# Kernel optimization log

Measured on AMD Instinct MI355X. Metric: run time of the kernel, lower is better.

## Reference

```python
import jax, jax.numpy as jnp
import numpy as np

B, H, W = 4, 128, 128
THRESHOLD = 0.1      # hard-coded in chamfer_distance_batch
CHUNK = 2048         # row-chunk size for the online-min over the distance matrix
BIG = 1e9            # masks out inactive columns in the min-reduction
EMPTY_CHD = 1e6      # sentinel when either point set is empty (matches torch code)
EPS = 1e-12          # sqrt clamp for numerical safety


def setup_inputs() -> dict:
    key = jax.random.key(0)
    k1, k2 = jax.random.split(key)
    batch1 = jax.random.normal(k1, (B, H, W), dtype=jnp.float32)
    batch2 = jax.random.normal(k2, (B, H, W), dtype=jnp.float32)
    return {"batch1": batch1, "batch2": batch2}


def _chamfer(batch1, batch2):
    Bn, Hn, Wn = batch1.shape
    HW = Hn * Wn
    w1 = jax.nn.relu(batch1 - THRESHOLD).reshape(Bn, HW)   # [B, HW]
    w2 = jax.nn.relu(batch2 - THRESHOLD).reshape(Bn, HW)
    gy, gx = jnp.meshgrid(jnp.arange(Hn), jnp.arange(Wn), indexing='ij')
    coords = jnp.stack([gy, gx], axis=-1).reshape(HW, 2).astype(jnp.float32)  # [HW, 2]
    # torch code multiplies coords by the relu'd weights BEFORE cdist (quirk kept)
    c1 = coords[None, :, :] * w1[:, :, None]               # [B, HW, 2]
    c2 = coords[None, :, :] * w2[:, :, None]
    m1 = w1 > 0                                            # active-point masks
    m2 = w2 > 0

    def directed(cf, mf, ct, mt):
        # mean over active rows of min distance to active columns, chunked
        ct_sq = jnp.sum(ct * ct, axis=-1)                  # [HW]

        def chunk_min(cc):                                 # cc: [CHUNK, 2]
            # |a-b|^2 = |a|^2 + |b|^2 - 2 a.b  (GEMM form)
            d2 = (jnp.sum(cc * cc, axis=-1)[:, None]
                  + ct_sq[None, :]
                  - 2.0 * cc @ ct.T)                       # [CHUNK, HW]
            d = jnp.sqrt(jnp.maximum(d2, EPS))
            return jnp.min(jnp.where(mt[None, :], d, BIG), axis=1)  # [CHUNK]

        mins = jax.lax.map(chunk_min, cf.reshape(-1, CHUNK, 2)).reshape(-1)  # [HW]
        n = jnp.sum(mf)
        return jnp.sum(mins * mf) / jnp.maximum(n, 1)

    def per_image(c1b, m1b, c2b, m2b):
        chd = directed(c1b, m1b, c2b, m2b) + directed(c2b, m2b, c1b, m1b)
        nonempty = (jnp.sum(m1b) > 0) & (jnp.sum(m2b) > 0)
        return jnp.where(nonempty, chd, jnp.asarray(EMPTY_CHD, chd.dtype))

    return jax.vmap(per_image)(c1, m1, c2, m2)   # [B]


def reference(batch1, batch2):
    return _chamfer(batch1, batch2)
```

## Files before the change

kernel.cpp:

```cpp
#include <hip/hip_runtime.h>
#include <math.h>


#define B_ 4
#define HW_ 16384
#define THRESH 0.1f
#define BIGF 1e30f
#define EPS_ 1e-12f

#define SEGCAP 4096
#define NSEG 4
#define NBIN 256
#define BINSCALE 0.25f
#define PD_NGRP 128

__global__ __launch_bounds__(1024)
void compact_kernel(const float* __restrict__ in1, const float* __restrict__ in2,
                    int* __restrict__ segcounts, float4* __restrict__ pts,
                    uint4* __restrict__ minarr4) {
    int seg = blockIdx.x, combo = blockIdx.y;
    int b = combo >> 1, s = combo & 1;
    int tid = threadIdx.x, lane = tid & 63, wid = tid >> 6;
    const float* in = s ? in2 : in1;
    int ibase = seg * SEGCAP + tid * 4;
    float4 v = ((const float4*)(in + b * HW_))[(unsigned)ibase >> 2];
    float w0 = v.x - THRESH, w1 = v.y - THRESH, w2 = v.z - THRESH, w3 = v.w - THRESH;
    int a0 = w0 > 0.f, a1 = w1 > 0.f, a2 = w2 > 0.f, a3 = w3 > 0.f;

    unsigned int bb = __float_as_uint(BIGF);
    minarr4[(unsigned)(combo * HW_ + ibase) >> 2] = make_uint4(bb, bb, bb, bb);

    int c = a0 + a1 + a2 + a3;
    int incl = c;
#pragma unroll
    for (int o = 1; o < 64; o <<= 1) {
        int x = __shfl_up(incl, o, 64);
        if (lane >= o) incl += x;
    }
    int wexcl = incl - c;
    __shared__ int wtot[16], wpre[17];
    if (lane == 63) wtot[wid] = incl;
    __syncthreads();
    if (tid == 0) {
        int run = 0;
#pragma unroll
        for (int ww = 0; ww < 16; ++ww) { wpre[ww] = run; run += wtot[ww]; }
        wpre[16] = run;
    }
    __syncthreads();
    int off = wpre[wid] + wexcl;
    float4* dst = pts + combo * HW_ + seg * SEGCAP;
    float wv[4] = {w0, w1, w2, w3};
    int   av[4] = {a0, a1, a2, a3};
#pragma unroll
    for (int u = 0; u < 4; ++u) {
        if (av[u]) {
            int i = ibase + u;
            float qx = (float)(i >> 7) * wv[u];
            float qy = (float)(i & 127) * wv[u];
            dst[off] = make_float4(qx, qy, qx * qx + qy * qy, 0.0f);
            ++off;
        }
    }
    if (tid == 0) segcounts[combo * 4 + seg] = wpre[16];
}

__global__ __launch_bounds__(1024)
void sort_kernel(const int* __restrict__ segcounts, const float4* __restrict__ pts,
                 float4* __restrict__ sorted, int* __restrict__ binstart) {
    int combo = blockIdx.x;
    int tid = threadIdx.x;
    __shared__ unsigned int hist[NBIN];
    __shared__ unsigned int cur[NBIN];
    if (tid < NBIN) hist[tid] = 0;
    __syncthreads();
    for (int s = 0; s < NSEG; ++s) {
        int c = segcounts[combo * 4 + s];
        const float4* seg = pts + combo * HW_ + s * SEGCAP;
        for (int i = tid; i < c; i += 1024) {
            float rho = sqrtf(seg[i].z);
            int bin = min(NBIN - 1, (int)(rho * BINSCALE));
            atomicAdd(&hist[bin], 1u);
        }
    }
    __syncthreads();
    if (tid == 0) {
        unsigned int run = 0;
        for (int bq = 0; bq < NBIN; ++bq) {
            cur[bq] = run;
            binstart[combo * (NBIN + 1) + bq] = (int)run;
            run += hist[bq];
        }
        binstart[combo * (NBIN + 1) + NBIN] = (int)run;
    }
    __syncthreads();
    for (int s = 0; s < NSEG; ++s) {
        int c = segcounts[combo * 4 + s];
        const float4* seg = pts + combo * HW_ + s * SEGCAP;
        for (int i = tid; i < c; i += 1024) {
            float4 p = seg[i];
            float rho = sqrtf(p.z);
            int bin = min(NBIN - 1, (int)(rho * BINSCALE));
            unsigned int idx = atomicAdd(&cur[bin], 1u);
            sorted[(size_t)combo * HW_ + idx] =
                make_float4(p.x, p.y, p.z, __uint_as_float((unsigned)(s * SEGCAP + i)));
        }
    }
}

__global__ __launch_bounds__(64)
void pdist_kernel(const float4* __restrict__ sorted, const int* __restrict__ binstart,
                  unsigned int* __restrict__ minarr) {
    int grp = blockIdx.x, combo = blockIdx.y;
    int lane = threadIdx.x;
    int tc = combo ^ 1;
    int n_from = binstart[combo * (NBIN + 1) + NBIN];
    int n_to   = binstart[tc * (NBIN + 1) + NBIN];
    if (n_from <= 0 || n_to <= 0) return;
    int rbase = grp * 128;
    if (rbase >= n_from) return;

    const float4* __restrict__ rows = sorted + (size_t)combo * HW_;
    const float4* __restrict__ cols = sorted + (size_t)tc * HW_;

    int r0 = rbase + lane, r1 = rbase + 64 + lane;
    bool v0 = r0 < n_from, v1 = r1 < n_from;
    float4 P0 = rows[min(r0, n_from - 1)];
    float4 P1 = rows[min(r1, n_from - 1)];
    float npx0 = -2.0f * P0.x, npy0 = -2.0f * P0.y, p20 = P0.z, rho0 = sqrtf(P0.z);
    float npx1 = -2.0f * P1.x, npy1 = -2.0f * P1.y, p21 = P1.z, rho1 = sqrtf(P1.z);
    unsigned int slot0 = __float_as_uint(P0.w);
    unsigned int slot1 = __float_as_uint(P1.w);
    float m0 = BIGF, m1 = BIGF;

    float rmid = sqrtf(rows[min(rbase + 64, n_from - 1)].z);
    int bmid = min(NBIN - 1, (int)(rmid * BINSCALE));
    int jlo = min(binstart[tc * (NBIN + 1) + bmid], n_to);
    int jhi = jlo;
    bool doneL = (jlo == 0), doneR = (jhi >= n_to);

    __shared__ __align__(16) float bufx[64];
    __shared__ __align__(16) float bufy[64];
    __shared__ __align__(16) float bufz[64];
    const float4* X = (const float4*)bufx;
    const float4* Y = (const float4*)bufy;
    const float4* Z = (const float4*)bufz;

    for (int iter = 0; (!doneL || !doneR) && iter < 2 * (HW_ / 64) + 4; ++iter) {
        bool left;
        if (doneL) left = false;
        else if (doneR) left = true;
        else left = (iter & 1);

        int jb = left ? (jlo - 64) : jhi;
        int j = jb + lane;
        float4 q = (j >= 0 && j < n_to) ? cols[j]
                                        : make_float4(0.0f, 0.0f, BIGF, 0.0f);
        bufx[lane] = q.x; bufy[lane] = q.y; bufz[lane] = q.z;
        __syncthreads();

#pragma unroll
        for (int q4 = 0; q4 < 16; ++q4) {
            float4 qx = X[q4], qy = Y[q4], qz = Z[q4];
            float t0 = fmaf(qy.x, npy0, fmaf(qx.x, npx0, qz.x));
            float u1 = fmaf(qy.y, npy0, fmaf(qx.y, npx0, qz.y));
            m0 = fminf(m0, fminf(t0, u1));
            float u2 = fmaf(qy.z, npy0, fmaf(qx.z, npx0, qz.z));
            float u3 = fmaf(qy.w, npy0, fmaf(qx.w, npx0, qz.w));
            m0 = fminf(m0, fminf(u2, u3));
            float s0 = fmaf(qy.x, npy1, fmaf(qx.x, npx1, qz.x));
            float s1 = fmaf(qy.y, npy1, fmaf(qx.y, npx1, qz.y));
            m1 = fminf(m1, fminf(s0, s1));
            float s2 = fmaf(qy.z, npy1, fmaf(qx.z, npx1, qz.z));
            float s3 = fmaf(qy.w, npy1, fmaf(qx.w, npx1, qz.w));
            m1 = fminf(m1, fminf(s2, s3));
        }
        __syncthreads();

        if (left) { jlo = max(jb, 0); doneL = doneL || (jlo == 0); }
        else      { jhi = min(jb + 64, n_to); doneR = doneR || (jhi >= n_to); }

        float md0 = v0 ? fmaxf(m0 + p20, 0.0f) : -1.0f;
        float md1 = v1 ? fmaxf(m1 + p21, 0.0f) : -1.0f;
        if (!doneL) {
            float reL = sqrtf(cols[jlo - 1].z);
            float d0 = rho0 - reL, d1 = rho1 - reL;
            bool pl0 = !v0 || ((rho0 > reL) && (d0 * d0 * 0.999f - 0.01f > md0));
            bool pl1 = !v1 || ((rho1 > reL) && (d1 * d1 * 0.999f - 0.01f > md1));
            doneL = __all(pl0 && pl1);
        }
        if (!doneR) {
            float reR = sqrtf(cols[jhi].z);
            float d0 = reR - rho0, d1 = reR - rho1;
            bool pr0 = !v0 || ((reR > rho0) && (d0 * d0 * 0.999f - 0.01f > md0));
            bool pr1 = !v1 || ((reR > rho1) && (d1 * d1 * 0.999f - 0.01f > md1));
            doneR = __all(pr0 && pr1);
        }
    }

    if (v0) minarr[combo * HW_ + slot0] = __float_as_uint(fmaxf(m0 + p20, 0.0f));
    if (v1) minarr[combo * HW_ + slot1] = __float_as_uint(fmaxf(m1 + p21, 0.0f));
}

__global__ void reduce_out_kernel(const int* __restrict__ segcounts,
                                  const unsigned int* __restrict__ minarr,
                                  float* __restrict__ out) {
    int b = blockIdx.x;
    int tid = threadIdx.x;
    int d = tid >> 9;
    int t = tid & 511;
    int combo = b * 2 + d;

    float acc = 0.0f;
    for (int s = 0; s < NSEG; ++s) {
        int c = segcounts[combo * 4 + s];
        const unsigned int* ma = minarr + combo * HW_ + s * SEGCAP;
        for (int r = t; r < c; r += 512)
            acc += sqrtf(fmaxf(__uint_as_float(ma[r]), EPS_));
    }
#pragma unroll
    for (int o = 32; o >= 1; o >>= 1) acc += __shfl_down(acc, o);

    __shared__ float wsum[16];
    if ((tid & 63) == 0) wsum[tid >> 6] = acc;
    __syncthreads();
    if (tid == 0) {
        float s0 = 0.0f, s1 = 0.0f;
#pragma unroll
        for (int w = 0; w < 8; ++w)  s0 += wsum[w];
#pragma unroll
        for (int w = 8; w < 16; ++w) s1 += wsum[w];
        int n0 = 0, n1 = 0;
#pragma unroll
        for (int s = 0; s < NSEG; ++s) {
            n0 += segcounts[(b * 2) * 4 + s];
            n1 += segcounts[(b * 2 + 1) * 4 + s];
        }
        out[b] = (n0 > 0 && n1 > 0)
                 ? s0 / (float)n0 + s1 / (float)n1
                 : 1.0e6f;
    }
}

extern "C" void kernel_launch(void* const* d_in, const int* in_sizes, int n_in,
                              void* d_out, int out_size, void* d_ws, size_t ws_size,
                              hipStream_t stream) {
    const float* in1 = (const float*)d_in[0];
    const float* in2 = (const float*)d_in[1];
    float* out = (float*)d_out;
    char* ws = (char*)d_ws;
    int* segcounts = (int*)ws;
    float4* pts = (float4*)(ws + 256);
    size_t minoff = 256 + (size_t)8 * HW_ * sizeof(float4);
    unsigned int* minarr = (unsigned int*)(ws + minoff);
    size_t sortoff = minoff + (size_t)8 * HW_ * sizeof(unsigned int);
    float4* sorted = (float4*)(ws + sortoff);
    size_t binoff = sortoff + (size_t)8 * HW_ * sizeof(float4);
    int* binstart = (int*)(ws + binoff);

    hipLaunchKernelGGL(compact_kernel, dim3(NSEG, 8), dim3(1024), 0, stream,
                       in1, in2, segcounts, pts, (uint4*)minarr);
    hipLaunchKernelGGL(sort_kernel, dim3(8), dim3(1024), 0, stream,
                       segcounts, pts, sorted, binstart);
    hipLaunchKernelGGL(pdist_kernel, dim3(PD_NGRP, 8), dim3(64), 0, stream,
                       sorted, binstart, minarr);
    hipLaunchKernelGGL(reduce_out_kernel, dim3(B_), dim3(1024), 0, stream,
                       segcounts, minarr, out);
}
```

Baseline: 96.00 us.

## Fuse histogram into compaction and parallelize bin scatter across segments

```diff
diff --git a/kernel.cpp b/kernel.cpp
--- a/kernel.cpp
+++ b/kernel.cpp
@@ -12,12 +12,13 @@
 #define NSEG 4
 #define NBIN 256
 #define BINSCALE 0.25f
+#define BINW 4.0f
 #define PD_NGRP 128
 
 __global__ __launch_bounds__(1024)
 void compact_kernel(const float* __restrict__ in1, const float* __restrict__ in2,
                     int* __restrict__ segcounts, float4* __restrict__ pts,
-                    uint4* __restrict__ minarr4) {
+                    uint4* __restrict__ minarr4, int* __restrict__ histG) {
     int seg = blockIdx.x, combo = blockIdx.y;
     int b = combo >> 1, s = combo & 1;
     int tid = threadIdx.x, lane = tid & 63, wid = tid >> 6;
@@ -30,6 +31,9 @@
     unsigned int bb = __float_as_uint(BIGF);
     minarr4[(unsigned)(combo * HW_ + ibase) >> 2] = make_uint4(bb, bb, bb, bb);
 
+    __shared__ int hist[NBIN];
+    if (tid < NBIN) hist[tid] = 0;
+
     int c = a0 + a1 + a2 + a3;
     int incl = c;
 #pragma unroll
@@ -58,53 +62,59 @@
             int i = ibase + u;
             float qx = (float)(i >> 7) * wv[u];
             float qy = (float)(i & 127) * wv[u];
-            dst[off] = make_float4(qx, qy, qx * qx + qy * qy, 0.0f);
+            float zz = qx * qx + qy * qy;
+            dst[off] = make_float4(qx, qy, zz, 0.0f);
+            int bin = min(NBIN - 1, (int)(sqrtf(zz) * BINSCALE));
+            atomicAdd(&hist[bin], 1);
             ++off;
         }
     }
     if (tid == 0) segcounts[combo * 4 + seg] = wpre[16];
-}
-
-__global__ __launch_bounds__(1024)
-void sort_kernel(const int* __restrict__ segcounts, const float4* __restrict__ pts,
-                 float4* __restrict__ sorted, int* __restrict__ binstart) {
-    int combo = blockIdx.x;
+    __syncthreads();
+    if (tid < NBIN)
+        histG[(combo * NSEG + seg) * NBIN + tid] = hist[tid];
+}
+
+__global__ __launch_bounds__(512)
+void scatter_kernel(const int* __restrict__ segcounts, const float4* __restrict__ pts,
+                    const int* __restrict__ histG, float4* __restrict__ sorted,
+                    int* __restrict__ binstartG) {
+    int seg = blockIdx.x, combo = blockIdx.y;
     int tid = threadIdx.x;
-    __shared__ unsigned int hist[NBIN];
-    __shared__ unsigned int cur[NBIN];
-    if (tid < NBIN) hist[tid] = 0;
-    __syncthreads();
-    for (int s = 0; s < NSEG; ++s) {
-        int c = segcounts[combo * 4 + s];
-        const float4* seg = pts + combo * HW_ + s * SEGCAP;
-        for (int i = tid; i < c; i += 1024) {
-            float rho = sqrtf(seg[i].z);
-            int bin = min(NBIN - 1, (int)(rho * BINSCALE));
-            atomicAdd(&hist[bin], 1u);
-        }
-    }
-    __syncthreads();
-    if (tid == 0) {
-        unsigned int run = 0;
-        for (int bq = 0; bq < NBIN; ++bq) {
-            cur[bq] = run;
-            binstart[combo * (NBIN + 1) + bq] = (int)run;
-            run += hist[bq];
-        }
-        binstart[combo * (NBIN + 1) + NBIN] = (int)run;
-    }
-    __syncthreads();
-    for (int s = 0; s < NSEG; ++s) {
-        int c = segcounts[combo * 4 + s];
-        const float4* seg = pts + combo * HW_ + s * SEGCAP;
-        for (int i = tid; i < c; i += 1024) {
-            float4 p = seg[i];
-            float rho = sqrtf(p.z);
-            int bin = min(NBIN - 1, (int)(rho * BINSCALE));
-            unsigned int idx = atomicAdd(&cur[bin], 1u);
-            sorted[(size_t)combo * HW_ + idx] =
-                make_float4(p.x, p.y, p.z, __uint_as_float((unsigned)(s * SEGCAP + i)));
-        }
+    __shared__ int h[NSEG][NBIN];
+    __shared__ int sc[NBIN];
+    __shared__ int cur[NBIN];
+    for (int i = tid; i < NSEG * NBIN; i += 512)
+        h[i >> 8][i & 255] = histG[combo * NSEG * NBIN + i];
+    __syncthreads();
+    if (tid < NBIN) sc[tid] = h[0][tid] + h[1][tid] + h[2][tid] + h[3][tid];
+    __syncthreads();
+#pragma unroll
+    for (int o = 1; o < NBIN; o <<= 1) {
+        int v = (tid < NBIN && tid >= o) ? sc[tid - o] : 0;
+        __syncthreads();
+        if (tid < NBIN) sc[tid] += v;
+        __syncthreads();
+    }
+    if (tid < NBIN) {
+        int tot = h[0][tid] + h[1][tid] + h[2][tid] + h[3][tid];
+        int excl = sc[tid] - tot;
+        int o2 = excl;
+        for (int s2 = 0; s2 < seg; ++s2) o2 += h[s2][tid];
+        cur[tid] = o2;
+        if (seg == 0) binstartG[combo * (NBIN + 1) + tid] = excl;
+    }
+    if (seg == 0 && tid == 0)
+        binstartG[combo * (NBIN + 1) + NBIN] = sc[NBIN - 1];
+    __syncthreads();
+    int c = segcounts[combo * 4 + seg];
+    const float4* src = pts + combo * HW_ + seg * SEGCAP;
+    for (int i = tid; i < c; i += 512) {
+        float4 p = src[i];
+        int bin = min(NBIN - 1, (int)(sqrtf(p.z) * BINSCALE));
+        int idx = atomicAdd(&cur[bin], 1);
+        sorted[(size_t)combo * HW_ + idx] =
+            make_float4(p.x, p.y, p.z, __uint_as_float((unsigned)(seg * SEGCAP + i)));
     }
 }
 
@@ -183,17 +193,19 @@
         float md0 = v0 ? fmaxf(m0 + p20, 0.0f) : -1.0f;
         float md1 = v1 ? fmaxf(m1 + p21, 0.0f) : -1.0f;
         if (!doneL) {
-            float reL = sqrtf(cols[jlo - 1].z);
-            float d0 = rho0 - reL, d1 = rho1 - reL;
-            bool pl0 = !v0 || ((rho0 > reL) && (d0 * d0 * 0.999f - 0.01f > md0));
-            bool pl1 = !v1 || ((rho1 > reL) && (d1 * d1 * 0.999f - 0.01f > md1));
+            int be = min(NBIN - 1, (int)(sqrtf(cols[jlo - 1].z) * BINSCALE));
+            float bndL = (float)(be + 1) * BINW;
+            float d0 = rho0 - bndL, d1 = rho1 - bndL;
+            bool pl0 = !v0 || ((d0 > 0.f) && (0.99f * d0 * d0 - 1.0f > md0));
+            bool pl1 = !v1 || ((d1 > 0.f) && (0.99f * d1 * d1 - 1.0f > md1));
             doneL = __all(pl0 && pl1);
         }
         if (!doneR) {
-            float reR = sqrtf(cols[jhi].z);
-            float d0 = reR - rho0, d1 = reR - rho1;
-            bool pr0 = !v0 || ((reR > rho0) && (d0 * d0 * 0.999f - 0.01f > md0));
-            bool pr1 = !v1 || ((reR > rho1) && (d1 * d1 * 0.999f - 0.01f > md1));
+            int be = (int)(sqrtf(cols[jhi].z) * BINSCALE);
+            float bndR = (float)be * BINW;
+            float d0 = bndR - rho0, d1 = bndR - rho1;
+            bool pr0 = !v0 || ((d0 > 0.f) && (0.99f * d0 * d0 - 1.0f > md0));
+            bool pr1 = !v1 || ((d1 > 0.f) && (0.99f * d1 * d1 - 1.0f > md1));
             doneR = __all(pr0 && pr1);
         }
     }
@@ -257,11 +269,13 @@
     float4* sorted = (float4*)(ws + sortoff);
     size_t binoff = sortoff + (size_t)8 * HW_ * sizeof(float4);
     int* binstart = (int*)(ws + binoff);
+    size_t histoff = binoff + (size_t)8 * (NBIN + 1) * sizeof(int);
+    int* histG = (int*)(ws + histoff);
 
     hipLaunchKernelGGL(compact_kernel, dim3(NSEG, 8), dim3(1024), 0, stream,
-                       in1, in2, segcounts, pts, (uint4*)minarr);
-    hipLaunchKernelGGL(sort_kernel, dim3(8), dim3(1024), 0, stream,
-                       segcounts, pts, sorted, binstart);
+                       in1, in2, segcounts, pts, (uint4*)minarr, histG);
+    hipLaunchKernelGGL(scatter_kernel, dim3(NSEG, 8), dim3(512), 0, stream,
+                       segcounts, pts, histG, sorted, binstart);
     hipLaunchKernelGGL(pdist_kernel, dim3(PD_NGRP, 8), dim3(64), 0, stream,
                        sorted, binstart, minarr);
     hipLaunchKernelGGL(reduce_out_kernel, dim3(B_), dim3(1024), 0, stream,
```

New measurement: 107.1 us. +11.6%, slower.
